# Kernel optimization log

Hardware: AMD Instinct MI355X
Metric: run time of the kernel (lower is better)

## Reference

```python
import jax, jax.numpy as jnp
import numpy as np

B = 1048576          # batch size
N_IN = 10            # input features
NQ = 3               # n_qubits
NM = 2               # n_fuzzy_mem
NC = NM ** NQ        # 8 fuzzy combinations
EPS_GN = 1e-5
EPS_BN = 1e-5
CLAMP = 0.99999

# bit pattern per combination: loc[j] is the j-th digit (MSB first) of i in binary
SEL = jnp.array([[(i >> 2) & 1, (i >> 1) & 1, i & 1] for i in range(NC)], dtype=jnp.int32)  # [8,3]


def setup_inputs() -> dict:
    key = jax.random.key(0)
    ks = jax.random.split(key, 12)
    x = jax.random.normal(ks[0], (B, N_IN), dtype=jnp.float32)
    # linear 10->3 (xavier-ish scale), bias init 0.01 per weights_init
    W1 = jax.random.normal(ks[1], (NQ, N_IN), dtype=jnp.float32) * (1.0 / np.sqrt(N_IN))
    b1 = jnp.full((NQ,), 0.01, dtype=jnp.float32)
    # GroupNorm(1,3) affine
    gamma = jnp.ones((NQ,), dtype=jnp.float32)
    beta = jnp.zeros((NQ,), dtype=jnp.float32)
    # fuzzy membership params m, theta ~ N(0,1), shape [n_qubits, n_fuzzy_mem]
    m = jax.random.normal(ks[2], (NQ, NM), dtype=jnp.float32)
    theta = jax.random.normal(ks[3], (NQ, NM), dtype=jnp.float32)
    # BatchNorm1d(8) affine
    gamma2 = jnp.ones((NC,), dtype=jnp.float32)
    beta2 = jnp.zeros((NC,), dtype=jnp.float32)
    # softmax_linear 8->10
    W2 = jax.random.normal(ks[4], (N_IN, NC), dtype=jnp.float32) * (1.0 / np.sqrt(NC))
    b2 = jnp.full((N_IN,), 0.01, dtype=jnp.float32)
    return {"x": x, "W1": W1, "b1": b1, "gamma": gamma, "beta": beta,
            "m": m, "theta": theta, "gamma2": gamma2, "beta2": beta2,
            "W2": W2, "b2": b2}


def reference(x, W1, b1, gamma, beta, m, theta, gamma2, beta2, W2, b2):
    # linear 10 -> 3
    h = x @ W1.T + b1                                   # [B,3]
    # GroupNorm(1,3): per-sample normalization over channels (biased var)
    mu = h.mean(axis=1, keepdims=True)
    var = ((h - mu) ** 2).mean(axis=1, keepdims=True)
    h = (h - mu) * jax.lax.rsqrt(var + EPS_GN) * gamma + beta
    # gaussian fuzzy memberships: [B, n_mem=2, n_qubits=3]
    mT = m.T[None]                                      # [1,2,3]
    tT = theta.T[None]                                  # [1,2,3]
    fuzzy = jnp.exp(-((h[:, None, :] - mT) ** 2) / (2.0 * tT ** 2))  # [B,2,3]
    # select membership per combination: q_in[b,i,j] = fuzzy[b, SEL[i,j], j]
    q_in = fuzzy[:, SEL, jnp.arange(NQ)]                # [B,8,3]
    # RY angle = 2*arcsin(clamp(sqrt(q+1e-16))); per-qubit P(|1>) = sin^2(angle/2)
    sq = jnp.clip(jnp.sqrt(q_in + 1e-16), None, CLAMP)
    p = sq * sq                                         # [B,8,3]
    # 5-qubit circuit RY,RY,RY + CCX(0,1,3) + CCX(2,3,4); probs[1] = P(q0=1,q1=0,q2=0)
    out = p[..., 0] * (1.0 - p[..., 1]) * (1.0 - p[..., 2])  # [B,8]
    # BatchNorm1d(8), training mode (batch stats, biased var)
    mu2 = out.mean(axis=0)
    var2 = ((out - mu2) ** 2).mean(axis=0)
    out = (out - mu2) * jax.lax.rsqrt(var2 + EPS_BN) * gamma2 + beta2
    # softmax_linear 8 -> 10
    logits = out @ W2.T + b2                            # [B,10]
    # q_defuzz: 3-qubit RY circuit on first 3 logits; probs[0..2]
    s = jnp.sin(logits[:, :NQ] * 0.5)
    pq = s * s                                          # P(q_i=1), [B,3]
    cq = 1.0 - pq
    res = jnp.stack([cq[:, 0] * cq[:, 1] * cq[:, 2],
                     pq[:, 0] * cq[:, 1] * cq[:, 2],
                     cq[:, 0] * pq[:, 1] * cq[:, 2]], axis=1)  # [B,3]
    return res
```

## Files before the change

### kernel.cpp

```cpp
#include <hip/hip_runtime.h>

#define NROWS 1048576
#define NPAIRS (NROWS / 2)
#define PMAX 0.9999800001f


__global__ void k_prep(const float* __restrict__ W1, const float* __restrict__ b1,
                       const float* __restrict__ gamma, const float* __restrict__ beta,
                       const float* __restrict__ m, const float* __restrict__ theta,
                       float* __restrict__ ws) {
    int t = threadIdx.x;
    if (t < 16) ws[t] = 0.0f;
    if (t < 30) ws[48 + t] = W1[t];
    if (t < 3) { ws[78 + t] = b1[t]; ws[81 + t] = gamma[t]; ws[84 + t] = beta[t]; }
    if (t < 6) { ws[87 + t] = m[t]; float th = theta[t]; ws[93 + t] = 1.0f / (2.0f * th * th); }
}

__device__ __forceinline__ void row_out(const float* xr, const float* __restrict__ wp,
                                        float* __restrict__ o) {
    float h0 = wp[78], h1 = wp[79], h2 = wp[80];
#pragma unroll
    for (int i = 0; i < 10; ++i) {
        h0 = fmaf(xr[i], wp[48 + i], h0);
        h1 = fmaf(xr[i], wp[58 + i], h1);
        h2 = fmaf(xr[i], wp[68 + i], h2);
    }
    float mu = (h0 + h1 + h2) * (1.0f / 3.0f);
    float d0 = h0 - mu, d1 = h1 - mu, d2 = h2 - mu;
    float var = (d0 * d0 + d1 * d1 + d2 * d2) * (1.0f / 3.0f);
    float rs = rsqrtf(var + 1e-5f);
    float hn[3];
    hn[0] = fmaf(d0 * rs, wp[81], wp[84]);
    hn[1] = fmaf(d1 * rs, wp[82], wp[85]);
    hn[2] = fmaf(d2 * rs, wp[83], wp[86]);
    float P[3][2];
#pragma unroll
    for (int q = 0; q < 3; ++q) {
#pragma unroll
        for (int s = 0; s < 2; ++s) {
            float d = hn[q] - wp[87 + q * 2 + s];
            float e = __expf(-(d * d) * wp[93 + q * 2 + s]);
            P[q][s] = fminf(e + 1e-16f, PMAX);
        }
    }
    float A0 = P[0][0], A1 = P[0][1];
    float B0 = 1.0f - P[1][0], B1 = 1.0f - P[1][1];
    float C0 = 1.0f - P[2][0], C1 = 1.0f - P[2][1];
    o[0] = A0 * B0 * C0; o[1] = A0 * B0 * C1; o[2] = A0 * B1 * C0; o[3] = A0 * B1 * C1;
    o[4] = A1 * B0 * C0; o[5] = A1 * B0 * C1; o[6] = A1 * B1 * C0; o[7] = A1 * B1 * C1;
}

#define P1_BLOCKS 512
#define P1_THREADS 256

__global__ __launch_bounds__(256) void k_pass1(const float* __restrict__ x,
                                               float* __restrict__ ws) {
    float s[8], ss[8];
#pragma unroll
    for (int c = 0; c < 8; ++c) { s[c] = 0.0f; ss[c] = 0.0f; }

    int tid = blockIdx.x * P1_THREADS + threadIdx.x;
    const int nthreads = P1_BLOCKS * P1_THREADS;
    for (int p = tid; p < NPAIRS; p += nthreads) {
        const float4* xv = reinterpret_cast<const float4*>(x) + (size_t)p * 5;
        float4 v0 = xv[0], v1 = xv[1], v2 = xv[2], v3 = xv[3], v4 = xv[4];
        float xr[20] = {v0.x, v0.y, v0.z, v0.w, v1.x, v1.y, v1.z, v1.w,
                        v2.x, v2.y, v2.z, v2.w, v3.x, v3.y, v3.z, v3.w,
                        v4.x, v4.y, v4.z, v4.w};
        float o[8];
        row_out(xr, ws, o);
#pragma unroll
        for (int c = 0; c < 8; ++c) { s[c] += o[c]; ss[c] = fmaf(o[c], o[c], ss[c]); }
        row_out(xr + 10, ws, o);
#pragma unroll
        for (int c = 0; c < 8; ++c) { s[c] += o[c]; ss[c] = fmaf(o[c], o[c], ss[c]); }
    }

#pragma unroll
    for (int c = 0; c < 8; ++c) {
#pragma unroll
        for (int off = 32; off > 0; off >>= 1) {
            s[c]  += __shfl_down(s[c], off);
            ss[c] += __shfl_down(ss[c], off);
        }
    }
    __shared__ float ls[4][16];
    int wave = threadIdx.x >> 6;
    if ((threadIdx.x & 63) == 0) {
#pragma unroll
        for (int c = 0; c < 8; ++c) { ls[wave][c] = s[c]; ls[wave][8 + c] = ss[c]; }
    }
    __syncthreads();
    if (threadIdx.x < 16) {
        float v = ls[0][threadIdx.x] + ls[1][threadIdx.x] + ls[2][threadIdx.x] + ls[3][threadIdx.x];
        atomicAdd(&ws[threadIdx.x], v);
    }
}

__global__ void k_finalize(const float* __restrict__ g2, const float* __restrict__ be2,
                           const float* __restrict__ W2, const float* __restrict__ b2,
                           float* __restrict__ ws) {
    __shared__ float a[8], sh[8];
    int t = threadIdx.x;
    if (t < 8) {
        const float invB = 1.0f / (float)NROWS;
        float mu = ws[t] * invB;
        float ex2 = ws[8 + t] * invB;
        float var = ex2 - mu * mu;
        float ac = g2[t] * rsqrtf(var + 1e-5f);
        a[t] = ac;
        sh[t] = be2[t] - mu * ac;
    }
    __syncthreads();
    if (t < 3) {
        float cst = b2[t];
#pragma unroll
        for (int c = 0; c < 8; ++c) {
            float w = W2[t * 8 + c];
            ws[16 + t * 8 + c] = w * a[c];
            cst += w * sh[c];
        }
        ws[40 + t] = cst;
    }
}

__global__ __launch_bounds__(256) void k_pass2(const float* __restrict__ x,
                                               const float* __restrict__ ws,
                                               float* __restrict__ res) {
    int p = blockIdx.x * 256 + threadIdx.x;
    const float4* xv = reinterpret_cast<const float4*>(x) + (size_t)p * 5;
    float4 v0 = xv[0], v1 = xv[1], v2 = xv[2], v3 = xv[3], v4 = xv[4];
    float xr[20] = {v0.x, v0.y, v0.z, v0.w, v1.x, v1.y, v1.z, v1.w,
                    v2.x, v2.y, v2.z, v2.w, v3.x, v3.y, v3.z, v3.w,
                    v4.x, v4.y, v4.z, v4.w};
    float r[6];
#pragma unroll
    for (int rr = 0; rr < 2; ++rr) {
        float o[8];
        row_out(xr + rr * 10, ws, o);
        float lg[3];
#pragma unroll
        for (int j = 0; j < 3; ++j) {
            float acc = ws[40 + j];
#pragma unroll
            for (int c = 0; c < 8; ++c) acc = fmaf(o[c], ws[16 + j * 8 + c], acc);
            lg[j] = acc;
        }
        float s0 = __sinf(0.5f * lg[0]), s1 = __sinf(0.5f * lg[1]), s2 = __sinf(0.5f * lg[2]);
        float pq0 = s0 * s0, pq1 = s1 * s1, pq2 = s2 * s2;
        float cq0 = 1.0f - pq0, cq1 = 1.0f - pq1, cq2 = 1.0f - pq2;
        r[rr * 3 + 0] = cq0 * cq1 * cq2;
        r[rr * 3 + 1] = pq0 * cq1 * cq2;
        r[rr * 3 + 2] = cq0 * pq1 * cq2;
    }
    float2* ro = reinterpret_cast<float2*>(res + (size_t)p * 6);
    ro[0] = make_float2(r[0], r[1]);
    ro[1] = make_float2(r[2], r[3]);
    ro[2] = make_float2(r[4], r[5]);
}

extern "C" void kernel_launch(void* const* d_in, const int* in_sizes, int n_in,
                              void* d_out, int out_size, void* d_ws, size_t ws_size,
                              hipStream_t stream) {
    const float* x     = (const float*)d_in[0];
    const float* W1    = (const float*)d_in[1];
    const float* b1    = (const float*)d_in[2];
    const float* gamma = (const float*)d_in[3];
    const float* beta  = (const float*)d_in[4];
    const float* m     = (const float*)d_in[5];
    const float* theta = (const float*)d_in[6];
    const float* g2    = (const float*)d_in[7];
    const float* be2   = (const float*)d_in[8];
    const float* W2    = (const float*)d_in[9];
    const float* b2    = (const float*)d_in[10];
    float* ws  = (float*)d_ws;
    float* res = (float*)d_out;

    hipLaunchKernelGGL(k_prep, dim3(1), dim3(64), 0, stream, W1, b1, gamma, beta, m, theta, ws);
    hipLaunchKernelGGL(k_pass1, dim3(P1_BLOCKS), dim3(P1_THREADS), 0, stream, x, ws);
    hipLaunchKernelGGL(k_finalize, dim3(1), dim3(64), 0, stream, g2, be2, W2, b2, ws);
    hipLaunchKernelGGL(k_pass2, dim3(NPAIRS / 256), dim3(256), 0, stream, x, ws, res);
}
```

Before: 117.4 us.

## Fold prep and finalize into passes, spread atomics, fold GroupNorm affine into fuzzy params

Removes the separate prep and finalize kernels. Each pass now builds its parameter table in shared memory, and pass2 computes the BatchNorm folding per block from the partial sums. Pass1 uses 1024 blocks with a fixed two-iteration loop, registers for the weights, and an LDS tree reduction. Its atomics are spread over 16 slots to cut contention. The GroupNorm gamma/beta are folded into the membership centre and width, which saves per-row FMAs but relies on gamma being nonzero; the workspace is zeroed with a memset.

```diff
diff --git a/kernel.cpp b/kernel.cpp
--- a/kernel.cpp
+++ b/kernel.cpp
@@ -1,48 +1,45 @@
 #include <hip/hip_runtime.h>
 
-#define NROWS 1048576
-#define NPAIRS (NROWS / 2)
-#define PMAX 0.9999800001f
-
-
-__global__ void k_prep(const float* __restrict__ W1, const float* __restrict__ b1,
-                       const float* __restrict__ gamma, const float* __restrict__ beta,
-                       const float* __restrict__ m, const float* __restrict__ theta,
-                       float* __restrict__ ws) {
-    int t = threadIdx.x;
-    if (t < 16) ws[t] = 0.0f;
-    if (t < 30) ws[48 + t] = W1[t];
-    if (t < 3) { ws[78 + t] = b1[t]; ws[81 + t] = gamma[t]; ws[84 + t] = beta[t]; }
-    if (t < 6) { ws[87 + t] = m[t]; float th = theta[t]; ws[93 + t] = 1.0f / (2.0f * th * th); }
-}
-
-__device__ __forceinline__ void row_out(const float* xr, const float* __restrict__ wp,
-                                        float* __restrict__ o) {
-    float h0 = wp[78], h1 = wp[79], h2 = wp[80];
+#define NROWS   1048576
+#define NPAIRS  (NROWS / 2)
+#define PMAX    0.9999800001f
+
+#define P1_BLOCKS 1024
+#define P1_THREADS 256
+#define P2_BLOCKS (NPAIRS / 256)
+
+__device__ __forceinline__ void fill_w(float* w, int t,
+        const float* __restrict__ W1, const float* __restrict__ b1,
+        const float* __restrict__ gamma, const float* __restrict__ beta,
+        const float* __restrict__ mm, const float* __restrict__ theta) {
+    if (t < 30) w[t] = W1[t];
+    else if (t < 33) w[t] = b1[t - 30];
+    else if (t < 39) { int k = t - 33; w[t] = (mm[k] - beta[k >> 1]) / gamma[k >> 1]; }
+    else if (t < 45) { int k = t - 39; float g = gamma[k >> 1], th = theta[k];
+                       w[t] = g * g / (2.0f * th * th); }
+}
+
+__device__ __forceinline__ void row_out(const float* xr, const float* w, float* o) {
+    float h0 = w[30], h1 = w[31], h2 = w[32];
 #pragma unroll
     for (int i = 0; i < 10; ++i) {
-        h0 = fmaf(xr[i], wp[48 + i], h0);
-        h1 = fmaf(xr[i], wp[58 + i], h1);
-        h2 = fmaf(xr[i], wp[68 + i], h2);
+        h0 = fmaf(xr[i], w[i],      h0);
+        h1 = fmaf(xr[i], w[10 + i], h1);
+        h2 = fmaf(xr[i], w[20 + i], h2);
     }
     float mu = (h0 + h1 + h2) * (1.0f / 3.0f);
     float d0 = h0 - mu, d1 = h1 - mu, d2 = h2 - mu;
-    float var = (d0 * d0 + d1 * d1 + d2 * d2) * (1.0f / 3.0f);
-    float rs = rsqrtf(var + 1e-5f);
-    float hn[3];
-    hn[0] = fmaf(d0 * rs, wp[81], wp[84]);
-    hn[1] = fmaf(d1 * rs, wp[82], wp[85]);
-    hn[2] = fmaf(d2 * rs, wp[83], wp[86]);
+    float rs = rsqrtf((d0 * d0 + d1 * d1 + d2 * d2) * (1.0f / 3.0f) + 1e-5f);
+    float u[3] = {d0 * rs, d1 * rs, d2 * rs};
     float P[3][2];
 #pragma unroll
-    for (int q = 0; q < 3; ++q) {
+    for (int q = 0; q < 3; ++q)
 #pragma unroll
         for (int s = 0; s < 2; ++s) {
-            float d = hn[q] - wp[87 + q * 2 + s];
-            float e = __expf(-(d * d) * wp[93 + q * 2 + s]);
+            float d = u[q] - w[33 + q * 2 + s];
+            float e = __expf(-(d * d) * w[39 + q * 2 + s]);
             P[q][s] = fminf(e + 1e-16f, PMAX);
         }
-    }
     float A0 = P[0][0], A1 = P[0][1];
     float B0 = 1.0f - P[1][0], B1 = 1.0f - P[1][1];
     float C0 = 1.0f - P[2][0], C1 = 1.0f - P[2][1];
@@ -50,100 +47,122 @@
     o[4] = A1 * B0 * C0; o[5] = A1 * B0 * C1; o[6] = A1 * B1 * C0; o[7] = A1 * B1 * C1;
 }
 
-#define P1_BLOCKS 512
-#define P1_THREADS 256
-
-__global__ __launch_bounds__(256) void k_pass1(const float* __restrict__ x,
-                                               float* __restrict__ ws) {
-    float s[8], ss[8];
-#pragma unroll
-    for (int c = 0; c < 8; ++c) { s[c] = 0.0f; ss[c] = 0.0f; }
-
-    int tid = blockIdx.x * P1_THREADS + threadIdx.x;
-    const int nthreads = P1_BLOCKS * P1_THREADS;
-    for (int p = tid; p < NPAIRS; p += nthreads) {
-        const float4* xv = reinterpret_cast<const float4*>(x) + (size_t)p * 5;
-        float4 v0 = xv[0], v1 = xv[1], v2 = xv[2], v3 = xv[3], v4 = xv[4];
-        float xr[20] = {v0.x, v0.y, v0.z, v0.w, v1.x, v1.y, v1.z, v1.w,
-                        v2.x, v2.y, v2.z, v2.w, v3.x, v3.y, v3.z, v3.w,
-                        v4.x, v4.y, v4.z, v4.w};
-        float o[8];
-        row_out(xr, ws, o);
-#pragma unroll
-        for (int c = 0; c < 8; ++c) { s[c] += o[c]; ss[c] = fmaf(o[c], o[c], ss[c]); }
-        row_out(xr + 10, ws, o);
-#pragma unroll
-        for (int c = 0; c < 8; ++c) { s[c] += o[c]; ss[c] = fmaf(o[c], o[c], ss[c]); }
-    }
-
-#pragma unroll
-    for (int c = 0; c < 8; ++c) {
-#pragma unroll
-        for (int off = 32; off > 0; off >>= 1) {
-            s[c]  += __shfl_down(s[c], off);
-            ss[c] += __shfl_down(ss[c], off);
-        }
-    }
-    __shared__ float ls[4][16];
-    int wave = threadIdx.x >> 6;
-    if ((threadIdx.x & 63) == 0) {
-#pragma unroll
-        for (int c = 0; c < 8; ++c) { ls[wave][c] = s[c]; ls[wave][8 + c] = ss[c]; }
-    }
-    __syncthreads();
-    if (threadIdx.x < 16) {
-        float v = ls[0][threadIdx.x] + ls[1][threadIdx.x] + ls[2][threadIdx.x] + ls[3][threadIdx.x];
-        atomicAdd(&ws[threadIdx.x], v);
-    }
-}
-
-__global__ void k_finalize(const float* __restrict__ g2, const float* __restrict__ be2,
-                           const float* __restrict__ W2, const float* __restrict__ b2,
-                           float* __restrict__ ws) {
-    __shared__ float a[8], sh[8];
-    int t = threadIdx.x;
-    if (t < 8) {
-        const float invB = 1.0f / (float)NROWS;
-        float mu = ws[t] * invB;
-        float ex2 = ws[8 + t] * invB;
-        float var = ex2 - mu * mu;
-        float ac = g2[t] * rsqrtf(var + 1e-5f);
-        a[t] = ac;
-        sh[t] = be2[t] - mu * ac;
-    }
-    __syncthreads();
-    if (t < 3) {
-        float cst = b2[t];
-#pragma unroll
-        for (int c = 0; c < 8; ++c) {
-            float w = W2[t * 8 + c];
-            ws[16 + t * 8 + c] = w * a[c];
-            cst += w * sh[c];
-        }
-        ws[40 + t] = cst;
-    }
-}
-
-__global__ __launch_bounds__(256) void k_pass2(const float* __restrict__ x,
-                                               const float* __restrict__ ws,
-                                               float* __restrict__ res) {
-    int p = blockIdx.x * 256 + threadIdx.x;
+__device__ __forceinline__ void load_pair(const float* __restrict__ x, int p, float* xr) {
     const float4* xv = reinterpret_cast<const float4*>(x) + (size_t)p * 5;
     float4 v0 = xv[0], v1 = xv[1], v2 = xv[2], v3 = xv[3], v4 = xv[4];
-    float xr[20] = {v0.x, v0.y, v0.z, v0.w, v1.x, v1.y, v1.z, v1.w,
-                    v2.x, v2.y, v2.z, v2.w, v3.x, v3.y, v3.z, v3.w,
-                    v4.x, v4.y, v4.z, v4.w};
+    xr[0] = v0.x; xr[1] = v0.y; xr[2] = v0.z; xr[3] = v0.w;
+    xr[4] = v1.x; xr[5] = v1.y; xr[6] = v1.z; xr[7] = v1.w;
+    xr[8] = v2.x; xr[9] = v2.y; xr[10] = v2.z; xr[11] = v2.w;
+    xr[12] = v3.x; xr[13] = v3.y; xr[14] = v3.z; xr[15] = v3.w;
+    xr[16] = v4.x; xr[17] = v4.y; xr[18] = v4.z; xr[19] = v4.w;
+}
+
+__global__ __launch_bounds__(256) void k_pass1(const float* __restrict__ x,
+        const float* __restrict__ W1, const float* __restrict__ b1,
+        const float* __restrict__ gamma, const float* __restrict__ beta,
+        const float* __restrict__ mm, const float* __restrict__ theta,
+        float* __restrict__ ws) {
+    __shared__ float w[45];
+    __shared__ float red[256][17];
+    __shared__ float red2[16][17];
+    int t = threadIdx.x;
+    fill_w(w, t, W1, b1, gamma, beta, mm, theta);
+    __syncthreads();
+
+    float rw[45];
+#pragma unroll
+    for (int i = 0; i < 45; ++i) rw[i] = w[i];
+
+    float s[8], ss[8];
+#pragma unroll
+    for (int c = 0; c < 8; ++c) { s[c] = 0.0f; ss[c] = 0.0f; }
+
+    int tid = blockIdx.x * P1_THREADS + t;
+    const int nthreads = P1_BLOCKS * P1_THREADS;
+#pragma unroll
+    for (int it = 0; it < 2; ++it) {
+        int p = tid + it * nthreads;
+        float xr[20];
+        load_pair(x, p, xr);
+        float o[8];
+        row_out(xr, rw, o);
+#pragma unroll
+        for (int c = 0; c < 8; ++c) { s[c] += o[c]; ss[c] = fmaf(o[c], o[c], ss[c]); }
+        row_out(xr + 10, rw, o);
+#pragma unroll
+        for (int c = 0; c < 8; ++c) { s[c] += o[c]; ss[c] = fmaf(o[c], o[c], ss[c]); }
+    }
+
+#pragma unroll
+    for (int c = 0; c < 8; ++c) { red[t][c] = s[c]; red[t][8 + c] = ss[c]; }
+    __syncthreads();
+    {
+        int c16 = t & 15, g = t >> 4;
+        float partial = 0.0f;
+#pragma unroll
+        for (int j = 0; j < 16; ++j) partial += red[g * 16 + j][c16];
+        red2[g][c16] = partial;
+    }
+    __syncthreads();
+    if (t < 16) {
+        float f = 0.0f;
+#pragma unroll
+        for (int g = 0; g < 16; ++g) f += red2[g][t];
+        atomicAdd(&ws[(blockIdx.x & 15) * 16 + t], f);
+    }
+}
+
+__global__ __launch_bounds__(256) void k_pass2(const float* __restrict__ x,
+        const float* __restrict__ W1, const float* __restrict__ b1,
+        const float* __restrict__ gamma, const float* __restrict__ beta,
+        const float* __restrict__ mm, const float* __restrict__ theta,
+        const float* __restrict__ g2, const float* __restrict__ be2,
+        const float* __restrict__ W2, const float* __restrict__ b2,
+        const float* __restrict__ ws, float* __restrict__ res) {
+    __shared__ float w[45];
+    __shared__ float weff[27];
+    __shared__ float a8[8], sh8[8];
+    int t = threadIdx.x;
+    fill_w(w, t, W1, b1, gamma, beta, mm, theta);
+    if (t >= 64 && t < 72) {
+        int c = t - 64;
+        float sv = 0.0f, qv = 0.0f;
+#pragma unroll
+        for (int r = 0; r < 16; ++r) { sv += ws[r * 16 + c]; qv += ws[r * 16 + 8 + c]; }
+        const float invB = 1.0f / (float)NROWS;
+        float mu = sv * invB;
+        float var = qv * invB - mu * mu;
+        float ac = g2[c] * rsqrtf(var + 1e-5f);
+        a8[c] = ac;
+        sh8[c] = be2[c] - mu * ac;
+    }
+    __syncthreads();
+    if (t < 3) {
+        float c0 = b2[t];
+#pragma unroll
+        for (int c = 0; c < 8; ++c) {
+            float wv = W2[t * 8 + c];
+            weff[t * 8 + c] = wv * a8[c];
+            c0 += wv * sh8[c];
+        }
+        weff[24 + t] = c0;
+    }
+    __syncthreads();
+
+    int p = blockIdx.x * 256 + t;
+    float xr[20];
+    load_pair(x, p, xr);
     float r[6];
 #pragma unroll
     for (int rr = 0; rr < 2; ++rr) {
         float o[8];
-        row_out(xr + rr * 10, ws, o);
+        row_out(xr + rr * 10, w, o);
         float lg[3];
 #pragma unroll
         for (int j = 0; j < 3; ++j) {
-            float acc = ws[40 + j];
-#pragma unroll
-            for (int c = 0; c < 8; ++c) acc = fmaf(o[c], ws[16 + j * 8 + c], acc);
+            float acc = weff[24 + j];
+#pragma unroll
+            for (int c = 0; c < 8; ++c) acc = fmaf(o[c], weff[j * 8 + c], acc);
             lg[j] = acc;
         }
         float s0 = __sinf(0.5f * lg[0]), s1 = __sinf(0.5f * lg[1]), s2 = __sinf(0.5f * lg[2]);
@@ -176,8 +195,9 @@
     float* ws  = (float*)d_ws;
     float* res = (float*)d_out;
 
-    hipLaunchKernelGGL(k_prep, dim3(1), dim3(64), 0, stream, W1, b1, gamma, beta, m, theta, ws);
-    hipLaunchKernelGGL(k_pass1, dim3(P1_BLOCKS), dim3(P1_THREADS), 0, stream, x, ws);
-    hipLaunchKernelGGL(k_finalize, dim3(1), dim3(64), 0, stream, g2, be2, W2, b2, ws);
-    hipLaunchKernelGGL(k_pass2, dim3(NPAIRS / 256), dim3(256), 0, stream, x, ws, res);
-}
+    hipMemsetAsync(ws, 0, 16 * 16 * sizeof(float), stream);
+    hipLaunchKernelGGL(k_pass1, dim3(P1_BLOCKS), dim3(P1_THREADS), 0, stream,
+                       x, W1, b1, gamma, beta, m, theta, ws);
+    hipLaunchKernelGGL(k_pass2, dim3(P2_BLOCKS), dim3(256), 0, stream,
+                       x, W1, b1, gamma, beta, m, theta, g2, be2, W2, b2, ws, res);
+}
```

After: 116.2 us. About the same (-1.1%).
